# Kernel tuning notes

Hardware: AMD Instinct MI355X
Metric: run time of the kernel (lower is better)

The kernel has to match this reference:

```python
import jax, jax.numpy as jnp
import numpy as np

N, E = 50000, 800000
D_IN, D_DEG, D_H, D_UP = 96, 32, 256, 128
EPS = 0.0  # non-trainable buffer, initial_eps=0


def setup_inputs() -> dict:
    key = jax.random.key(0)
    ks = jax.random.split(key, 8)
    d = D_IN + D_DEG  # 128, feature dim after degree-as-tag concat
    return {
        "x": jax.random.normal(ks[0], (N, D_IN), dtype=jnp.float32),
        "degrees": jax.random.uniform(ks[1], (N, D_DEG), dtype=jnp.float32),
        "edge_features": jax.random.normal(ks[2], (E, d), dtype=jnp.float32),
        "W1": jax.random.normal(ks[3], (d, D_H), dtype=jnp.float32) * (1.0 / np.sqrt(d)),
        "b1": jnp.zeros((D_H,), dtype=jnp.float32),
        "W2": jax.random.normal(ks[4], (D_H, D_UP), dtype=jnp.float32) * (1.0 / np.sqrt(D_H)),
        "b2": jnp.zeros((D_UP,), dtype=jnp.float32),
        "edge_index": jax.random.randint(ks[5], (2, E), 0, N, dtype=jnp.int64),
    }


def reference(x, degrees, edge_features, W1, b1, W2, b2, edge_index):
    # degree_as_tag + retain_features: concat node features with degree tags
    h = jnp.concatenate([x, degrees], axis=-1)  # [N, 128]
    # flow='source_to_target': source j = edge_index[0], target i = edge_index[1]
    src, dst = edge_index[0], edge_index[1]
    msgs = jax.nn.relu(h[src] + edge_features)  # [E, 128]
    agg = jax.ops.segment_sum(msgs, dst, num_segments=N)  # [N, 128]
    z = (1.0 + EPS) * h + agg
    # update MLP: Linear -> ReLU -> Linear
    out = jax.nn.relu(z @ W1 + b1) @ W2 + b2  # [N, 128]
    return out
```

## Files before the change

### kernel.cpp

```cpp
#include <hip/hip_runtime.h>


constexpr int DIN  = 96;
constexpr int DDEG = 32;
constexpr int D    = 128;
constexpr int DH   = 256;
constexpr int DUP  = 128;

typedef short bf16x8 __attribute__((ext_vector_type(8)));
typedef float f32x4  __attribute__((ext_vector_type(4)));

static __device__ __forceinline__ ushort f2bf(float f) {
    unsigned u = __float_as_uint(f);
    unsigned r = (u + 0x7fff + ((u >> 16) & 1)) >> 16;
    return (ushort)r;
}

static __device__ __forceinline__ int waveInclScan(int v, int lane) {
#pragma unroll
    for (int off = 1; off < 64; off <<= 1) {
        int t = __shfl_up(v, off, 64);
        if (lane >= off) v += t;
    }
    return v;
}

__global__ __launch_bounds__(256) void count_kernel(
    const int* __restrict__ ei, int* __restrict__ counts, int N, int E) {
    int e = blockIdx.x * 256 + threadIdx.x;
    if (e >= E) return;
    atomicAdd(&counts[ei[E + e]], 1);
}

__global__ __launch_bounds__(256) void scan_partial_kernel(
    const int* __restrict__ counts, int* __restrict__ blockSums, int N) {
    const int tid = threadIdx.x;
    int base = blockIdx.x * 1024 + tid * 4;
    int4 c = make_int4(0, 0, 0, 0);
    if (base + 3 < N) c = *reinterpret_cast<const int4*>(&counts[base]);
    else if (base < N) {
        c.x = counts[base];
        if (base + 1 < N) c.y = counts[base + 1];
        if (base + 2 < N) c.z = counts[base + 2];
    }
    int s = c.x + c.y + c.z + c.w;
#pragma unroll
    for (int off = 32; off; off >>= 1) s += __shfl_xor(s, off, 64);
    __shared__ int wsum[4];
    if ((tid & 63) == 0) wsum[tid >> 6] = s;
    __syncthreads();
    if (tid == 0) blockSums[blockIdx.x] = wsum[0] + wsum[1] + wsum[2] + wsum[3];
}

__global__ __launch_bounds__(64) void scan_base_kernel(
    const int* __restrict__ blockSums, int* __restrict__ blockBase, int nb) {
    int l = threadIdx.x;
    int orig = (l < nb) ? blockSums[l] : 0;
    int incl = waveInclScan(orig, l);
    if (l < nb) blockBase[l] = incl - orig;
}

__global__ __launch_bounds__(256) void scan_final_kernel(
    const int* __restrict__ counts, const int* __restrict__ blockBase,
    int* __restrict__ offsets, int* __restrict__ cursor, int N, int E) {
    const int tid = threadIdx.x, lane = tid & 63, wave = tid >> 6;
    int base = blockIdx.x * 1024 + tid * 4;
    int4 c = make_int4(0, 0, 0, 0);
    if (base + 3 < N) c = *reinterpret_cast<const int4*>(&counts[base]);
    else if (base < N) {
        c.x = counts[base];
        if (base + 1 < N) c.y = counts[base + 1];
        if (base + 2 < N) c.z = counts[base + 2];
    }
    int s = c.x + c.y + c.z + c.w;
    int incl = waveInclScan(s, lane);
    __shared__ int wsum[4];
    if (lane == 63) wsum[wave] = incl;
    __syncthreads();
    int wb = 0;
#pragma unroll
    for (int w = 0; w < 4; ++w)
        if (w < wave) wb += wsum[w];
    int ex = blockBase[blockIdx.x] + wb + (incl - s);
    if (base < N)     { offsets[base]     = ex; cursor[base]     = ex; } ex += c.x;
    if (base + 1 < N) { offsets[base + 1] = ex; cursor[base + 1] = ex; } ex += c.y;
    if (base + 2 < N) { offsets[base + 2] = ex; cursor[base + 2] = ex; } ex += c.z;
    if (base + 3 < N) { offsets[base + 3] = ex; cursor[base + 3] = ex; }
    if (blockIdx.x == 0 && tid == 0) offsets[N] = E;
}

__global__ __launch_bounds__(256) void fill_kernel(
    const int* __restrict__ ei, int* __restrict__ cursor,
    int* __restrict__ eids, int E) {
    int e = blockIdx.x * 256 + threadIdx.x;
    if (e >= E) return;
    int pos = atomicAdd(&cursor[ei[E + e]], 1);
    eids[pos] = e;
}

__global__ __launch_bounds__(256) void gather_kernel(
    const float* __restrict__ x, const float* __restrict__ deg,
    const float* __restrict__ ef, const int* __restrict__ ei,
    const int* __restrict__ offsets, const int* __restrict__ eids,
    ushort* __restrict__ zb, int N, int E) {
    const int node = blockIdx.x * 8 + (threadIdx.x >> 5);
    if (node >= N) return;
    const int c = threadIdx.x & 31;

    float4 h;
    if (c < 24) h = *reinterpret_cast<const float4*>(&x[(size_t)node * DIN + c * 4]);
    else        h = *reinterpret_cast<const float4*>(&deg[(size_t)node * DDEG + (c - 24) * 4]);

    float4 acc = make_float4(0.f, 0.f, 0.f, 0.f);
    const int pBeg = offsets[node], pEnd = offsets[node + 1];
    int e_nxt = 0, src_nxt = 0;
    if (pBeg < pEnd) { e_nxt = eids[pBeg]; src_nxt = ei[e_nxt]; }
    for (int p = pBeg; p < pEnd; ++p) {
        int e = e_nxt, src = src_nxt;
        if (p + 1 < pEnd) { e_nxt = eids[p + 1]; src_nxt = ei[e_nxt]; }
        float4 fv = *reinterpret_cast<const float4*>(&ef[(size_t)e * D + c * 4]);
        float4 hs;
        if (c < 24) hs = *reinterpret_cast<const float4*>(&x[(size_t)src * DIN + c * 4]);
        else        hs = *reinterpret_cast<const float4*>(&deg[(size_t)src * DDEG + (c - 24) * 4]);
        acc.x += fmaxf(fv.x + hs.x, 0.f);
        acc.y += fmaxf(fv.y + hs.y, 0.f);
        acc.z += fmaxf(fv.z + hs.z, 0.f);
        acc.w += fmaxf(fv.w + hs.w, 0.f);
    }
    ushort4 o;
    o.x = f2bf(h.x + acc.x);
    o.y = f2bf(h.y + acc.y);
    o.z = f2bf(h.z + acc.z);
    o.w = f2bf(h.w + acc.w);
    *reinterpret_cast<ushort4*>(&zb[(size_t)node * D + c * 4]) = o;
}

__global__ __launch_bounds__(256) void pack_w_kernel(
    const float* __restrict__ W1, const float* __restrict__ W2,
    ushort* __restrict__ w1p, ushort* __restrict__ w2p) {
    int idx = blockIdx.x * 256 + threadIdx.x;
    if (idx >= 32768) return;
    {
        int j = idx & 7, l = (idx >> 3) & 63, nb = (idx >> 9) & 15, kb = idx >> 13;
        int k = kb * 32 + (l >> 4) * 8 + j, n = nb * 16 + (l & 15);
        w1p[idx] = f2bf(W1[k * DH + n]);
    }
    {
        int j = idx & 7, l = (idx >> 3) & 63, nb = (idx >> 9) & 7, kb = idx >> 12;
        int k = kb * 32 + (l >> 4) * 8 + j, n = nb * 16 + (l & 15);
        w2p[idx] = f2bf(W2[k * DUP + n]);
    }
}

__global__ __launch_bounds__(256) void mlp_mfma_kernel(
    const ushort* __restrict__ zb,
    const ushort* __restrict__ w1p, const float* __restrict__ b1,
    const ushort* __restrict__ w2p, const float* __restrict__ b2,
    float* __restrict__ out, int N) {
    __shared__ ushort u_lds[4][16][DH + 8];
    const int tid = threadIdx.x;
    const int wave = tid >> 6, lane = tid & 63;
    const int m0 = blockIdx.x * 64 + wave * 16;
    const int lr = lane & 15, lg = lane >> 4;

    bf16x8 a1[4];
    int rowA = m0 + lr; if (rowA > N - 1) rowA = N - 1;
    const ushort* zrow = &zb[(size_t)rowA * D + lg * 8];
#pragma unroll
    for (int kb = 0; kb < 4; ++kb)
        a1[kb] = *reinterpret_cast<const bf16x8*>(zrow + kb * 32);

#pragma unroll
    for (int nb = 0; nb < 16; ++nb) {
        f32x4 c = {0.f, 0.f, 0.f, 0.f};
#pragma unroll
        for (int kb = 0; kb < 4; ++kb) {
            bf16x8 b = *reinterpret_cast<const bf16x8*>(&w1p[((kb * 16 + nb) * 64 + lane) * 8]);
            c = __builtin_amdgcn_mfma_f32_16x16x32_bf16(a1[kb], b, c, 0, 0, 0);
        }
        float bias = b1[nb * 16 + lr];
#pragma unroll
        for (int r = 0; r < 4; ++r) {
            float v = fmaxf(c[r] + bias, 0.f);
            u_lds[wave][lg * 4 + r][nb * 16 + lr] = f2bf(v);
        }
    }
    __syncthreads();

    bf16x8 a2[8];
#pragma unroll
    for (int kb = 0; kb < 8; ++kb)
        a2[kb] = *reinterpret_cast<const bf16x8*>(&u_lds[wave][lr][kb * 32 + lg * 8]);

#pragma unroll
    for (int nb = 0; nb < 8; ++nb) {
        f32x4 c = {0.f, 0.f, 0.f, 0.f};
#pragma unroll
        for (int kb = 0; kb < 8; ++kb) {
            bf16x8 b = *reinterpret_cast<const bf16x8*>(&w2p[((kb * 8 + nb) * 64 + lane) * 8]);
            c = __builtin_amdgcn_mfma_f32_16x16x32_bf16(a2[kb], b, c, 0, 0, 0);
        }
        float bias = b2[nb * 16 + lr];
#pragma unroll
        for (int r = 0; r < 4; ++r) {
            int row = m0 + lg * 4 + r;
            if (row < N) out[(size_t)row * DUP + nb * 16 + lr] = c[r] + bias;
        }
    }
}

extern "C" void kernel_launch(void* const* d_in, const int* in_sizes, int n_in,
                              void* d_out, int out_size, void* d_ws, size_t ws_size,
                              hipStream_t stream) {
    const float* x   = (const float*)d_in[0];
    const float* dg  = (const float*)d_in[1];
    const float* ef  = (const float*)d_in[2];
    const float* W1  = (const float*)d_in[3];
    const float* b1  = (const float*)d_in[4];
    const float* W2  = (const float*)d_in[5];
    const float* b2  = (const float*)d_in[6];
    const int*   ei  = (const int*)d_in[7];
    float* out = (float*)d_out;

    const int N = in_sizes[0] / DIN;
    const int E = in_sizes[7] / 2;

    auto align16 = [](size_t v) { return (v + 15) & ~(size_t)15; };
    char* w = (char*)d_ws;
    ushort* zb      = (ushort*)w;  w += align16((size_t)N * D * 2);
    int*   counts   = (int*)w;     w += align16((size_t)N * 4);
    int*   offsets  = (int*)w;     w += align16((size_t)(N + 1) * 4);
    int*   cursor   = (int*)w;     w += align16((size_t)N * 4);
    int*   eids     = (int*)w;     w += align16((size_t)E * 4);
    int*   blockSums= (int*)w;     w += align16(64 * 4);
    int*   blockBase= (int*)w;     w += align16(64 * 4);
    ushort* w1p     = (ushort*)w;  w += align16((size_t)D * DH * 2);
    ushort* w2p     = (ushort*)w;  w += align16((size_t)DH * DUP * 2);

    hipMemsetAsync(counts, 0, (size_t)N * 4, stream);

    const int eb = (E + 255) / 256;
    const int nbScan = (N + 1023) / 1024;

    count_kernel<<<eb, 256, 0, stream>>>(ei, counts, N, E);
    scan_partial_kernel<<<nbScan, 256, 0, stream>>>(counts, blockSums, N);
    scan_base_kernel<<<1, 64, 0, stream>>>(blockSums, blockBase, nbScan);
    scan_final_kernel<<<nbScan, 256, 0, stream>>>(counts, blockBase, offsets, cursor, N, E);
    fill_kernel<<<eb, 256, 0, stream>>>(ei, cursor, eids, E);

    gather_kernel<<<(N + 7) / 8, 256, 0, stream>>>(x, dg, ef, ei, offsets, eids, zb, N, E);

    pack_w_kernel<<<128, 256, 0, stream>>>(W1, W2, w1p, w2p);
    mlp_mfma_kernel<<<(N + 63) / 64, 256, 0, stream>>>(zb, w1p, b1, w2p, b2, out, N);
}
```

Baseline: 291.5 us.

## Pack source ids with edge ids, gather bf16 node features, split edges across half-waves

```diff
diff --git a/kernel.cpp b/kernel.cpp
--- a/kernel.cpp
+++ b/kernel.cpp
@@ -15,6 +15,14 @@
     unsigned r = (u + 0x7fff + ((u >> 16) & 1)) >> 16;
     return (ushort)r;
 }
+static __device__ __forceinline__ float4 bf4_to_f4(ushort4 u) {
+    float4 r;
+    r.x = __uint_as_float((unsigned)u.x << 16);
+    r.y = __uint_as_float((unsigned)u.y << 16);
+    r.z = __uint_as_float((unsigned)u.z << 16);
+    r.w = __uint_as_float((unsigned)u.w << 16);
+    return r;
+}
 
 static __device__ __forceinline__ int waveInclScan(int v, int lane) {
 #pragma unroll
@@ -23,6 +31,20 @@
         if (lane >= off) v += t;
     }
     return v;
+}
+
+__global__ __launch_bounds__(256) void init_h_kernel(
+    const float* __restrict__ x, const float* __restrict__ deg,
+    ushort* __restrict__ hp, int N) {
+    int t = blockIdx.x * 256 + threadIdx.x;
+    if (t >= N * 32) return;
+    int n = t >> 5, c = t & 31;
+    float4 v;
+    if (c < 24) v = *reinterpret_cast<const float4*>(&x[(size_t)n * DIN + c * 4]);
+    else        v = *reinterpret_cast<const float4*>(&deg[(size_t)n * DDEG + (c - 24) * 4]);
+    ushort4 o;
+    o.x = f2bf(v.x); o.y = f2bf(v.y); o.z = f2bf(v.z); o.w = f2bf(v.w);
+    *reinterpret_cast<ushort4*>(&hp[(size_t)n * D + c * 4]) = o;
 }
 
 __global__ __launch_bounds__(256) void count_kernel(
@@ -91,48 +113,66 @@
 
 __global__ __launch_bounds__(256) void fill_kernel(
     const int* __restrict__ ei, int* __restrict__ cursor,
-    int* __restrict__ eids, int E) {
+    int2* __restrict__ eids2, int E) {
     int e = blockIdx.x * 256 + threadIdx.x;
     if (e >= E) return;
-    int pos = atomicAdd(&cursor[ei[E + e]], 1);
-    eids[pos] = e;
+    int src = ei[e];
+    int dst = ei[E + e];
+    int pos = atomicAdd(&cursor[dst], 1);
+    eids2[pos] = make_int2(e, src);
 }
 
 __global__ __launch_bounds__(256) void gather_kernel(
-    const float* __restrict__ x, const float* __restrict__ deg,
-    const float* __restrict__ ef, const int* __restrict__ ei,
-    const int* __restrict__ offsets, const int* __restrict__ eids,
-    ushort* __restrict__ zb, int N, int E) {
-    const int node = blockIdx.x * 8 + (threadIdx.x >> 5);
+    const ushort* __restrict__ hp, const float* __restrict__ ef,
+    const int* __restrict__ offsets, const int2* __restrict__ eids2,
+    ushort* __restrict__ zb, int N) {
+    const int wave = threadIdx.x >> 6, lane = threadIdx.x & 63;
+    const int node = blockIdx.x * 4 + wave;
     if (node >= N) return;
-    const int c = threadIdx.x & 31;
-
-    float4 h;
-    if (c < 24) h = *reinterpret_cast<const float4*>(&x[(size_t)node * DIN + c * 4]);
-    else        h = *reinterpret_cast<const float4*>(&deg[(size_t)node * DDEG + (c - 24) * 4]);
+    const int c = lane & 31;
+    const int eh = lane >> 5;
+
+    float4 h = bf4_to_f4(*reinterpret_cast<const ushort4*>(&hp[(size_t)node * D + c * 4]));
 
     float4 acc = make_float4(0.f, 0.f, 0.f, 0.f);
     const int pBeg = offsets[node], pEnd = offsets[node + 1];
-    int e_nxt = 0, src_nxt = 0;
-    if (pBeg < pEnd) { e_nxt = eids[pBeg]; src_nxt = ei[e_nxt]; }
-    for (int p = pBeg; p < pEnd; ++p) {
-        int e = e_nxt, src = src_nxt;
-        if (p + 1 < pEnd) { e_nxt = eids[p + 1]; src_nxt = ei[e_nxt]; }
-        float4 fv = *reinterpret_cast<const float4*>(&ef[(size_t)e * D + c * 4]);
-        float4 hs;
-        if (c < 24) hs = *reinterpret_cast<const float4*>(&x[(size_t)src * DIN + c * 4]);
-        else        hs = *reinterpret_cast<const float4*>(&deg[(size_t)src * DDEG + (c - 24) * 4]);
-        acc.x += fmaxf(fv.x + hs.x, 0.f);
-        acc.y += fmaxf(fv.y + hs.y, 0.f);
-        acc.z += fmaxf(fv.z + hs.z, 0.f);
-        acc.w += fmaxf(fv.w + hs.w, 0.f);
-    }
-    ushort4 o;
-    o.x = f2bf(h.x + acc.x);
-    o.y = f2bf(h.y + acc.y);
-    o.z = f2bf(h.z + acc.z);
-    o.w = f2bf(h.w + acc.w);
-    *reinterpret_cast<ushort4*>(&zb[(size_t)node * D + c * 4]) = o;
+    int p = pBeg + eh;
+    for (; p + 2 < pEnd; p += 4) {
+        int2 ea = eids2[p];
+        int2 eb = eids2[p + 2];
+        f32x4 f0 = __builtin_nontemporal_load(
+            reinterpret_cast<const f32x4*>(&ef[(size_t)ea.x * D + c * 4]));
+        f32x4 f1 = __builtin_nontemporal_load(
+            reinterpret_cast<const f32x4*>(&ef[(size_t)eb.x * D + c * 4]));
+        float4 h0 = bf4_to_f4(*reinterpret_cast<const ushort4*>(&hp[(size_t)ea.y * D + c * 4]));
+        float4 h1 = bf4_to_f4(*reinterpret_cast<const ushort4*>(&hp[(size_t)eb.y * D + c * 4]));
+        acc.x += fmaxf(f0[0] + h0.x, 0.f) + fmaxf(f1[0] + h1.x, 0.f);
+        acc.y += fmaxf(f0[1] + h0.y, 0.f) + fmaxf(f1[1] + h1.y, 0.f);
+        acc.z += fmaxf(f0[2] + h0.z, 0.f) + fmaxf(f1[2] + h1.z, 0.f);
+        acc.w += fmaxf(f0[3] + h0.w, 0.f) + fmaxf(f1[3] + h1.w, 0.f);
+    }
+    for (; p < pEnd; p += 2) {
+        int2 ea = eids2[p];
+        f32x4 f0 = __builtin_nontemporal_load(
+            reinterpret_cast<const f32x4*>(&ef[(size_t)ea.x * D + c * 4]));
+        float4 h0 = bf4_to_f4(*reinterpret_cast<const ushort4*>(&hp[(size_t)ea.y * D + c * 4]));
+        acc.x += fmaxf(f0[0] + h0.x, 0.f);
+        acc.y += fmaxf(f0[1] + h0.y, 0.f);
+        acc.z += fmaxf(f0[2] + h0.z, 0.f);
+        acc.w += fmaxf(f0[3] + h0.w, 0.f);
+    }
+    acc.x += __shfl_xor(acc.x, 32, 64);
+    acc.y += __shfl_xor(acc.y, 32, 64);
+    acc.z += __shfl_xor(acc.z, 32, 64);
+    acc.w += __shfl_xor(acc.w, 32, 64);
+    if (eh == 0) {
+        ushort4 o;
+        o.x = f2bf(h.x + acc.x);
+        o.y = f2bf(h.y + acc.y);
+        o.z = f2bf(h.z + acc.z);
+        o.w = f2bf(h.w + acc.w);
+        *reinterpret_cast<ushort4*>(&zb[(size_t)node * D + c * 4]) = o;
+    }
 }
 
 __global__ __launch_bounds__(256) void pack_w_kernel(
@@ -228,10 +268,11 @@
     auto align16 = [](size_t v) { return (v + 15) & ~(size_t)15; };
     char* w = (char*)d_ws;
     ushort* zb      = (ushort*)w;  w += align16((size_t)N * D * 2);
+    ushort* hp      = (ushort*)w;  w += align16((size_t)N * D * 2);
     int*   counts   = (int*)w;     w += align16((size_t)N * 4);
     int*   offsets  = (int*)w;     w += align16((size_t)(N + 1) * 4);
     int*   cursor   = (int*)w;     w += align16((size_t)N * 4);
-    int*   eids     = (int*)w;     w += align16((size_t)E * 4);
+    int2*  eids2    = (int2*)w;    w += align16((size_t)E * 8);
     int*   blockSums= (int*)w;     w += align16(64 * 4);
     int*   blockBase= (int*)w;     w += align16(64 * 4);
     ushort* w1p     = (ushort*)w;  w += align16((size_t)D * DH * 2);
@@ -242,13 +283,14 @@
     const int eb = (E + 255) / 256;
     const int nbScan = (N + 1023) / 1024;
 
+    init_h_kernel<<<(N * 32 + 255) / 256, 256, 0, stream>>>(x, dg, hp, N);
     count_kernel<<<eb, 256, 0, stream>>>(ei, counts, N, E);
     scan_partial_kernel<<<nbScan, 256, 0, stream>>>(counts, blockSums, N);
     scan_base_kernel<<<1, 64, 0, stream>>>(blockSums, blockBase, nbScan);
     scan_final_kernel<<<nbScan, 256, 0, stream>>>(counts, blockBase, offsets, cursor, N, E);
-    fill_kernel<<<eb, 256, 0, stream>>>(ei, cursor, eids, E);
-
-    gather_kernel<<<(N + 7) / 8, 256, 0, stream>>>(x, dg, ef, ei, offsets, eids, zb, N, E);
+    fill_kernel<<<eb, 256, 0, stream>>>(ei, cursor, eids2, E);
+
+    gather_kernel<<<(N + 3) / 4, 256, 0, stream>>>(hp, ef, offsets, eids2, zb, N);
 
     pack_w_kernel<<<128, 256, 0, stream>>>(W1, W2, w1p, w2p);
     mlp_mfma_kernel<<<(N + 63) / 64, 256, 0, stream>>>(zb, w1p, b1, w2p, b2, out, N);
```

New measurement: 249.2 us. 1.17x faster.
